# Performance work log

Hardware: AMD Instinct MI355X
Metric: run time of the kernel (lower is better)

The kernel has to match this reference:

```python
import jax, jax.numpy as jnp
import numpy as np

DIM = 32      # feature dim (must be small: unnormalized det prod overflows fp32 otherwise)
K = 16        # number of mixture components / experts
B = 262144    # batch


def setup_inputs() -> dict:
    key = jax.random.key(0)
    k0, k1, k2, k3, k4 = jax.random.split(key, 5)
    x = jax.random.normal(k0, (B, DIM), dtype=jnp.float32)
    xavier = 1.0 / np.sqrt(DIM / 2.0)
    mu = (jax.random.normal(k1, (K, DIM), dtype=jnp.float32) * xavier)
    # torch init is ones; use small values so prod(2*pi*sigma2) stays finite in fp32
    logsigma = jax.random.normal(k2, (K, DIM), dtype=jnp.float32) * 0.1
    W = jax.random.normal(k3, (K, DIM, DIM), dtype=jnp.float32) * (1.0 / np.sqrt(DIM))
    b = jax.random.normal(k4, (K, DIM), dtype=jnp.float32) * 0.01
    return {"x": x, "mu": mu, "logsigma": logsigma, "W": W, "b": b}


def reference(x, mu, logsigma, W, b):
    # Gaussian prior pdf per expert, vectorized over k
    two_pi = np.float32(2.0 * np.pi)
    sigma2 = jnp.exp(2.0 * logsigma)                                   # [k, d]
    const = jax.lax.rsqrt(jnp.prod(two_pi * sigma2, axis=-1))           # [k]
    diff = x[None, :, :] - mu[:, None, :]                               # [k, b, d]
    exponent = -0.5 * jnp.sum(diff * diff / sigma2[:, None, :], axis=-1)  # [k, b]
    ps = const[:, None] * jnp.exp(exponent)                             # [k, b]
    w = ps / jnp.sum(ps, axis=0, keepdims=True)                         # [k, b]
    # per-expert Linear (torch convention: x @ W_k.T + b_k) + ReLU
    lik = jax.nn.relu(jnp.einsum('bd,kod->kbo', x, W) + b[:, None, :])  # [k, b, d]
    # gate-weighted sum over experts
    return jnp.einsum('kb,kbo->bo', w, lik)                             # [b, d]
```

## Files before the change

### kernel.cpp

```cpp
#include <hip/hip_runtime.h>
#include <math.h>

#define DIM 32
#define NK  16
#define LOG2E 1.4426950408889634f

typedef __attribute__((ext_vector_type(8))) short bf16x8;
typedef __attribute__((ext_vector_type(4))) float f32x4;

#define MFMA16 __builtin_amdgcn_mfma_f32_16x16x32_bf16

#define WHI_OFF 0
#define WLO_OFF 32768
#define HH_OFF  65536
#define HL_OFF  66560
#define GH_OFF  67584
#define GL_OFF  68608
#define CG_OFF  69632

typedef __attribute__((address_space(1))) const unsigned int gu32;
typedef __attribute__((address_space(3))) unsigned int lu32;

__device__ __forceinline__ void split2(float x, short* hi, short* lo) {
  unsigned u = __float_as_uint(x);
  *hi = (short)(u >> 16);
  float hf = __uint_as_float(u & 0xFFFF0000u);
  float l = x - hf;
  *lo = (short)(__float_as_uint(l) >> 16);
}

__global__ __launch_bounds__(256) void gmm_setup_kernel(
    const float* __restrict__ mu, const float* __restrict__ logsigma,
    const float* __restrict__ W, char* __restrict__ ws)
{
  int i = blockIdx.x * 256 + threadIdx.x;
  short* whi = (short*)(ws + WHI_OFF);
  short* wlo = (short*)(ws + WLO_OFF);
  if (i < NK * DIM * DIM) split2(W[i], &whi[i], &wlo[i]);
  if (i < NK * DIM) {
    float s2 = __expf(2.0f * logsigma[i]);
    float h = (-0.5f / s2) * LOG2E;
    float g = (mu[i] / s2) * LOG2E;
    short a, b;
    split2(h, &a, &b);
    ((short*)(ws + HH_OFF))[i] = a; ((short*)(ws + HL_OFF))[i] = b;
    split2(g, &a, &b);
    ((short*)(ws + GH_OFF))[i] = a; ((short*)(ws + GL_OFF))[i] = b;
  }
  if (i < NK) {
    float acc = 0.0f;
    for (int d = 0; d < DIM; ++d) {
      float s2 = __expf(2.0f * logsigma[i * DIM + d]);
      float m  = mu[i * DIM + d];
      acc += m * m * (-0.5f / s2) * LOG2E - 0.5f * log2f(6.283185307179586f * s2);
    }
    ((float*)(ws + CG_OFF))[i] = acc;
  }
}

__global__ __launch_bounds__(256, 3) void gmm_moe_kernel(
    const float* __restrict__ x,
    const float* __restrict__ bias,
    const char* __restrict__ ws,
    float* __restrict__ out)
{
  __shared__ char  lds_w[32768];
  __shared__ float lds_p[4][4][NK][16];
  const int tid  = threadIdx.x;
  const int wid  = tid >> 6;
  const int lane = tid & 63;
  const int g = lane >> 4;
  const int c = lane & 15;
  const int sbase = (blockIdx.x * 4 + wid) * 64;

  float4 xa[4][2];
  #pragma unroll
  for (int t = 0; t < 4; ++t) {
    const float4* xp =
        (const float4*)(x + (size_t)(sbase + t * 16 + c) * DIM + g * 8);
    xa[t][0] = xp[0];
    xa[t][1] = xp[1];
  }

  const bf16x8 fhh = ((const bf16x8*)(ws + HH_OFF))[c * 4 + g];
  const bf16x8 fhl = ((const bf16x8*)(ws + HL_OFF))[c * 4 + g];
  const bf16x8 fgh = ((const bf16x8*)(ws + GH_OFF))[c * 4 + g];
  const bf16x8 fgl = ((const bf16x8*)(ws + GL_OFF))[c * 4 + g];
  const float  cgv = ((const float*)(ws + CG_OFF))[c];

  #pragma unroll
  for (int i = 0; i < 8; ++i) {
    int off = wid * 8192 + i * 1024;
    __builtin_amdgcn_global_load_lds(
        (gu32*)(ws + WHI_OFF + off + lane * 16),
        (lu32*)(lds_w + off), 16, 0, 0);
  }

  bf16x8 xh[4], xl[4];
  #pragma unroll
  for (int t = 0; t < 4; ++t) {
    float xv[8] = {xa[t][0].x, xa[t][0].y, xa[t][0].z, xa[t][0].w,
                   xa[t][1].x, xa[t][1].y, xa[t][1].z, xa[t][1].w};
    bf16x8 x2h, x2l;
    #pragma unroll
    for (int j = 0; j < 8; ++j) {
      short h_, l_;
      split2(xv[j], &h_, &l_);
      xh[t][j] = h_; xl[t][j] = l_;
      float q = xv[j] * xv[j];
      split2(q, &h_, &l_);
      x2h[j] = h_; x2l[j] = l_;
    }
    f32x4 e = {cgv, cgv, cgv, cgv};
    e = MFMA16(x2h,   fhh, e, 0, 0, 0);
    e = MFMA16(x2l,   fhh, e, 0, 0, 0);
    e = MFMA16(x2h,   fhl, e, 0, 0, 0);
    e = MFMA16(xh[t], fgh, e, 0, 0, 0);
    e = MFMA16(xl[t], fgh, e, 0, 0, 0);
    e = MFMA16(xh[t], fgl, e, 0, 0, 0);
    float pr[4], sr[4];
    #pragma unroll
    for (int r = 0; r < 4; ++r) {
      pr[r] = __builtin_amdgcn_exp2f(e[r]);
      float s = pr[r];
      s += __shfl_xor(s, 1, 64);
      s += __shfl_xor(s, 2, 64);
      s += __shfl_xor(s, 4, 64);
      s += __shfl_xor(s, 8, 64);
      sr[r] = s;
    }
    f32x4 wv;
    #pragma unroll
    for (int r = 0; r < 4; ++r) wv[r] = pr[r] * __builtin_amdgcn_rcpf(sr[r]);
    *(f32x4*)&lds_p[wid][t][c][g * 4] = wv;
  }

  __syncthreads();

  const bf16x8* wlo = (const bf16x8*)(ws + WLO_OFF);
  f32x4 o0[4], o1[4];
  #pragma unroll
  for (int t = 0; t < 4; ++t) { o0[t] = (f32x4){0,0,0,0}; o1[t] = (f32x4){0,0,0,0}; }

  #pragma unroll
  for (int k = 0; k < NK; ++k) {
    const bf16x8 w0h = *(const bf16x8*)(lds_w + k * 2048 + c * 64 + g * 16);
    const bf16x8 w1h = *(const bf16x8*)(lds_w + k * 2048 + (16 + c) * 64 + g * 16);
    const bf16x8 w0l = wlo[(k * DIM +      c) * 4 + g];
    const bf16x8 w1l = wlo[(k * DIM + 16 + c) * 4 + g];
    const float b0 = bias[k * DIM + c];
    const float b1 = bias[k * DIM + 16 + c];
    #pragma unroll
    for (int t = 0; t < 4; ++t) {
      f32x4 s0 = {b0, b0, b0, b0}, s1 = {b1, b1, b1, b1};
      s0 = MFMA16(xh[t], w0h, s0, 0, 0, 0);
      s0 = MFMA16(xl[t], w0h, s0, 0, 0, 0);
      s0 = MFMA16(xh[t], w0l, s0, 0, 0, 0);
      s1 = MFMA16(xh[t], w1h, s1, 0, 0, 0);
      s1 = MFMA16(xl[t], w1h, s1, 0, 0, 0);
      s1 = MFMA16(xh[t], w1l, s1, 0, 0, 0);
      const f32x4 wv = *(const f32x4*)&lds_p[wid][t][k][g * 4];
      const f32x4 z = {0.0f, 0.0f, 0.0f, 0.0f};
      o0[t] = __builtin_elementwise_fma(wv, __builtin_elementwise_max(s0, z), o0[t]);
      o1[t] = __builtin_elementwise_fma(wv, __builtin_elementwise_max(s1, z), o1[t]);
    }
  }

  #pragma unroll
  for (int t = 0; t < 4; ++t) {
    #pragma unroll
    for (int r = 0; r < 4; ++r) {
      size_t row = (size_t)(sbase + t * 16 + g * 4 + r);
      out[row * DIM + c]      = o0[t][r];
      out[row * DIM + 16 + c] = o1[t][r];
    }
  }
}

extern "C" void kernel_launch(void* const* d_in, const int* in_sizes, int n_in,
                              void* d_out, int out_size, void* d_ws, size_t ws_size,
                              hipStream_t stream) {
  const float* x  = (const float*)d_in[0];
  const float* mu = (const float*)d_in[1];
  const float* ls = (const float*)d_in[2];
  const float* W  = (const float*)d_in[3];
  const float* bv = (const float*)d_in[4];
  float* out = (float*)d_out;
  const int B = in_sizes[0] / DIM;

  gmm_setup_kernel<<<(NK * DIM * DIM + 255) / 256, 256, 0, stream>>>(
      mu, ls, W, (char*)d_ws);
  gmm_moe_kernel<<<B / 256, 256, 0, stream>>>(x, bv, (const char*)d_ws, out);
}
```

Measured before the change: 114.9 us.

## Stage both W halves in LDS, use 512-thread blocks, broadcast gates via shuffles

Blocks now have 8 waves of 32 rows each instead of 4 waves of 64 rows. The low-part W is staged into LDS alongside the high part (64KB), so its per-iteration global loads go away. The gate weights stay in registers and are broadcast with cross-lane shuffles instead of going through an LDS scratch array. This cuts global traffic and register pressure per wave and raises the wave count. The cost is more LDS per block, which may limit occupancy, and extra shuffle instructions in the inner loop.

```diff
diff --git a/kernel.cpp b/kernel.cpp
--- a/kernel.cpp
+++ b/kernel.cpp
@@ -58,24 +58,30 @@
   }
 }
 
-__global__ __launch_bounds__(256, 3) void gmm_moe_kernel(
+__global__ __launch_bounds__(512, 4) void gmm_moe_kernel(
     const float* __restrict__ x,
     const float* __restrict__ bias,
     const char* __restrict__ ws,
     float* __restrict__ out)
 {
-  __shared__ char  lds_w[32768];
-  __shared__ float lds_p[4][4][NK][16];
+  __shared__ char lds_w[65536];
   const int tid  = threadIdx.x;
   const int wid  = tid >> 6;
   const int lane = tid & 63;
   const int g = lane >> 4;
   const int c = lane & 15;
-  const int sbase = (blockIdx.x * 4 + wid) * 64;
+  const int sbase = (blockIdx.x * 8 + wid) * 32;
 
-  float4 xa[4][2];
   #pragma unroll
-  for (int t = 0; t < 4; ++t) {
+  for (int r = 0; r < 8; ++r) {
+    const int off = r * 8192 + wid * 1024;
+    __builtin_amdgcn_global_load_lds(
+        (gu32*)(ws + off + lane * 16), (lu32*)(lds_w + off), 16, 0, 0);
+  }
+
+  float4 xa[2][2];
+  #pragma unroll
+  for (int t = 0; t < 2; ++t) {
     const float4* xp =
         (const float4*)(x + (size_t)(sbase + t * 16 + c) * DIM + g * 8);
     xa[t][0] = xp[0];
@@ -88,17 +94,10 @@
   const bf16x8 fgl = ((const bf16x8*)(ws + GL_OFF))[c * 4 + g];
   const float  cgv = ((const float*)(ws + CG_OFF))[c];
 
+  bf16x8 xh[2], xl[2];
+  f32x4 wv[2];
   #pragma unroll
-  for (int i = 0; i < 8; ++i) {
-    int off = wid * 8192 + i * 1024;
-    __builtin_amdgcn_global_load_lds(
-        (gu32*)(ws + WHI_OFF + off + lane * 16),
-        (lu32*)(lds_w + off), 16, 0, 0);
-  }
-
-  bf16x8 xh[4], xl[4];
-  #pragma unroll
-  for (int t = 0; t < 4; ++t) {
+  for (int t = 0; t < 2; ++t) {
     float xv[8] = {xa[t][0].x, xa[t][0].y, xa[t][0].z, xa[t][0].w,
                    xa[t][1].x, xa[t][1].y, xa[t][1].z, xa[t][1].w};
     bf16x8 x2h, x2l;
@@ -118,40 +117,35 @@
     e = MFMA16(xh[t], fgh, e, 0, 0, 0);
     e = MFMA16(xl[t], fgh, e, 0, 0, 0);
     e = MFMA16(xh[t], fgl, e, 0, 0, 0);
-    float pr[4], sr[4];
     #pragma unroll
     for (int r = 0; r < 4; ++r) {
-      pr[r] = __builtin_amdgcn_exp2f(e[r]);
-      float s = pr[r];
+      float p = __builtin_amdgcn_exp2f(e[r]);
+      float s = p;
       s += __shfl_xor(s, 1, 64);
       s += __shfl_xor(s, 2, 64);
       s += __shfl_xor(s, 4, 64);
       s += __shfl_xor(s, 8, 64);
-      sr[r] = s;
+      wv[t][r] = p * __builtin_amdgcn_rcpf(s);
     }
-    f32x4 wv;
-    #pragma unroll
-    for (int r = 0; r < 4; ++r) wv[r] = pr[r] * __builtin_amdgcn_rcpf(sr[r]);
-    *(f32x4*)&lds_p[wid][t][c][g * 4] = wv;
   }
 
   __syncthreads();
 
-  const bf16x8* wlo = (const bf16x8*)(ws + WLO_OFF);
-  f32x4 o0[4], o1[4];
+  f32x4 o0[2], o1[2];
   #pragma unroll
-  for (int t = 0; t < 4; ++t) { o0[t] = (f32x4){0,0,0,0}; o1[t] = (f32x4){0,0,0,0}; }
+  for (int t = 0; t < 2; ++t) { o0[t] = (f32x4){0,0,0,0}; o1[t] = (f32x4){0,0,0,0}; }
 
+  const int wbase = c * 64 + g * 16;
   #pragma unroll
   for (int k = 0; k < NK; ++k) {
-    const bf16x8 w0h = *(const bf16x8*)(lds_w + k * 2048 + c * 64 + g * 16);
-    const bf16x8 w1h = *(const bf16x8*)(lds_w + k * 2048 + (16 + c) * 64 + g * 16);
-    const bf16x8 w0l = wlo[(k * DIM +      c) * 4 + g];
-    const bf16x8 w1l = wlo[(k * DIM + 16 + c) * 4 + g];
+    const bf16x8 w0h = *(const bf16x8*)(lds_w + k * 2048 + wbase);
+    const bf16x8 w1h = *(const bf16x8*)(lds_w + k * 2048 + 1024 + wbase);
+    const bf16x8 w0l = *(const bf16x8*)(lds_w + 32768 + k * 2048 + wbase);
+    const bf16x8 w1l = *(const bf16x8*)(lds_w + 32768 + k * 2048 + 1024 + wbase);
     const float b0 = bias[k * DIM + c];
     const float b1 = bias[k * DIM + 16 + c];
     #pragma unroll
-    for (int t = 0; t < 4; ++t) {
+    for (int t = 0; t < 2; ++t) {
       f32x4 s0 = {b0, b0, b0, b0}, s1 = {b1, b1, b1, b1};
       s0 = MFMA16(xh[t], w0h, s0, 0, 0, 0);
       s0 = MFMA16(xl[t], w0h, s0, 0, 0, 0);
@@ -159,15 +153,18 @@
       s1 = MFMA16(xh[t], w1h, s1, 0, 0, 0);
       s1 = MFMA16(xl[t], w1h, s1, 0, 0, 0);
       s1 = MFMA16(xh[t], w1l, s1, 0, 0, 0);
-      const f32x4 wv = *(const f32x4*)&lds_p[wid][t][k][g * 4];
+      f32x4 wb;
+      #pragma unroll
+      for (int r = 0; r < 4; ++r)
+        wb[r] = __shfl(wv[t][r], (lane & 48) | k, 64);
       const f32x4 z = {0.0f, 0.0f, 0.0f, 0.0f};
-      o0[t] = __builtin_elementwise_fma(wv, __builtin_elementwise_max(s0, z), o0[t]);
-      o1[t] = __builtin_elementwise_fma(wv, __builtin_elementwise_max(s1, z), o1[t]);
+      o0[t] = __builtin_elementwise_fma(wb, __builtin_elementwise_max(s0, z), o0[t]);
+      o1[t] = __builtin_elementwise_fma(wb, __builtin_elementwise_max(s1, z), o1[t]);
     }
   }
 
   #pragma unroll
-  for (int t = 0; t < 4; ++t) {
+  for (int t = 0; t < 2; ++t) {
     #pragma unroll
     for (int r = 0; r < 4; ++r) {
       size_t row = (size_t)(sbase + t * 16 + g * 4 + r);
@@ -190,5 +187,5 @@
 
   gmm_setup_kernel<<<(NK * DIM * DIM + 255) / 256, 256, 0, stream>>>(
       mu, ls, W, (char*)d_ws);
-  gmm_moe_kernel<<<B / 256, 256, 0, stream>>>(x, bv, (const char*)d_ws, out);
+  gmm_moe_kernel<<<B / 256, 512, 0, stream>>>(x, bv, (const char*)d_ws, out);
 }
```

New measurement: 117.4 us. 1.02x slower.
